# Performance work log

Hardware: AMD Instinct MI355X
Metric: run time of the kernel (lower is better)

The kernel has to match this reference:

```python
import jax, jax.numpy as jnp
import numpy as np

TOPK_FRAC = 0.05  # init arg `topk` (fraction of pool kept)


def setup_inputs() -> dict:
    key = jax.random.key(0)
    k1, k2 = jax.random.split(key)
    x = jax.random.normal(k1, (16, 256, 32, 32), dtype=jnp.float32)
    # nn.Parameter(torch.rand(P, C)) -> uniform [0, 1)
    visual_concept_pool = jax.random.uniform(k2, (2048, 256), dtype=jnp.float32)
    return {"x": x, "visual_concept_pool": visual_concept_pool}


def reference(x, visual_concept_pool):
    n, c, h, w = x.shape
    P = visual_concept_pool.shape[0]
    L = h * w
    xf = x.reshape(n, c, L)                              # [n, c, L]
    # dot_product[n, P, L] = pool @ xf
    dot = jnp.einsum('pc,ncl->npl', visual_concept_pool, xf)
    pool_norm = jnp.sqrt(jnp.sum(visual_concept_pool ** 2, axis=1))   # [P]
    x_norm = jnp.sqrt(jnp.sum(xf ** 2, axis=1))                        # [n, L]
    cos = dot / (pool_norm[None, :, None] * x_norm[:, None, :])       # [n, P, L]

    # mode 1.1: top-k over the pool dimension per (n, pixel)
    keep = int(TOPK_FRAC * P)
    cos_t = jnp.transpose(cos, (0, 2, 1))                # [n, L, P]
    _, idx = jax.lax.top_k(jnp.abs(cos_t), keep)         # [n, L, keep]
    mask = jnp.zeros_like(cos_t).at[
        jnp.arange(n)[:, None, None],
        jnp.arange(L)[None, :, None],
        idx,
    ].set(1.0)                                           # [n, L, P]
    masked = cos_t * mask
    normed = masked / jnp.sum(masked, axis=-1, keepdims=True)  # renormalize over P
    # reconstruct[n, c, L] = pool^T @ cos
    recon = jnp.einsum('pc,nlp->ncl', visual_concept_pool, normed)
    return recon.reshape(n, c, h, w)
```

## Files before the change

### kernel.cpp

```cpp
#include <hip/hip_runtime.h>
#include <hip/hip_fp16.h>

typedef unsigned short u16;
typedef _Float16 half8 __attribute__((ext_vector_type(8)));
typedef float floatx4 __attribute__((ext_vector_type(4)));

#define C_DIM 256
#define P_DIM 2048
#define L_DIM 1024
#define N_DIM 16
#define KEEP 102
#define KPAD 104
#define HALF_PIX 8192
#define SCALE 256.0f

__device__ __forceinline__ void st8(u16* dst, const u16* s) {
  uint4 u;
  u.x = (unsigned)s[0] | ((unsigned)s[1] << 16);
  u.y = (unsigned)s[2] | ((unsigned)s[3] << 16);
  u.z = (unsigned)s[4] | ((unsigned)s[5] << 16);
  u.w = (unsigned)s[6] | ((unsigned)s[7] << 16);
  *(uint4*)dst = u;
}

__device__ __forceinline__ u16 f2h_ftz(float v) {
  if (fabsf(v) < 6.103515625e-5f) return 0;
  return __half_as_ushort(__float2half(v));
}

__device__ __forceinline__ void gl_lds16(const u16* g, u16* l) {
  __builtin_amdgcn_global_load_lds(
      (const __attribute__((address_space(1))) unsigned int*)g,
      (__attribute__((address_space(3))) unsigned int*)l, 16, 0, 0);
}

__global__ __launch_bounds__(256) void k_pinv(const float* __restrict__ pool,
                                              float* __restrict__ pinv) {
  int p = blockIdx.x * 256 + threadIdx.x;
  const float4* row = (const float4*)(pool + (size_t)p * C_DIM);
  float s = 0.f;
#pragma unroll
  for (int i = 0; i < C_DIM / 4; ++i) {
    float4 v = row[i];
    s += v.x * v.x + v.y * v.y + v.z * v.z + v.w * v.w;
  }
  pinv[p] = 1.0f / sqrtf(s);
}

__global__ __launch_bounds__(256) void k_packpool(const float* __restrict__ pool,
                                                  const float* __restrict__ pinv,
                                                  u16* __restrict__ ah,
                                                  u16* __restrict__ al,
                                                  u16* __restrict__ ph) {
  int tid = blockIdx.x * 256 + threadIdx.x;
  int lane = tid & 63;
  int ks = (tid >> 6) & 7;
  int pm = tid >> 9;
  int p = pm * 16 + (lane & 15);
  int c0 = ks * 32 + ((lane >> 4) << 3);
  float sc = pinv[p] * SCALE;
  const float* src = pool + (size_t)p * C_DIM + c0;
  u16 h8[8], l8[8], p8[8];
#pragma unroll
  for (int j = 0; j < 8; ++j) {
    float raw = src[j];
    p8[j] = __half_as_ushort(__float2half(raw));
    float v = raw * sc;
    u16 h = f2h_ftz(v);
    float r = v - __half2float(__ushort_as_half(h));
    h8[j] = h;
    l8[j] = f2h_ftz(r);
  }
  size_t o = (size_t)tid * 8;
  st8(ah + o, h8); st8(al + o, l8);
  st8(ph + (size_t)p * C_DIM + c0, p8);
}

__global__ __launch_bounds__(256) void k_packx(const float* __restrict__ x,
                                               u16* __restrict__ xh,
                                               u16* __restrict__ xl) {
  int tid = blockIdx.x * 256 + threadIdx.x;
  int lane = tid & 63;
  int ks = (tid >> 6) & 7;
  int pn = tid >> 9;
  int pix = pn * 16 + (lane & 15);
  int n = pix >> 10, l = pix & 1023;
  int c0 = ks * 32 + ((lane >> 4) << 3);
  const float* src = x + ((size_t)(n * C_DIM + c0)) * L_DIM + l;
  u16 h8[8], l8[8];
#pragma unroll
  for (int j = 0; j < 8; ++j) {
    float v = src[(size_t)j * L_DIM] * SCALE;
    u16 h = f2h_ftz(v);
    float r = v - __half2float(__ushort_as_half(h));
    h8[j] = h;
    l8[j] = f2h_ftz(r);
  }
  size_t o = (size_t)tid * 8;
  st8(xh + o, h8); st8(xl + o, l8);
}

__global__ __launch_bounds__(256, 4) void k_mfma(const u16* __restrict__ ah_,
                                                 const u16* __restrict__ al_,
                                                 const u16* __restrict__ xh_,
                                                 const u16* __restrict__ xl_,
                                                 float* __restrict__ sbuf,
                                                 int half) {
  __shared__ u16 sB[2][2][8][512];

  const int t = threadIdx.x, lane = t & 63, w = t >> 6;
  const int pT = blockIdx.x & 15, pixT = blockIdx.x >> 4;
  const int pmBase = pT * 8 + w * 2;
  const int pnBase = half * 512 + pixT * 8;
  const half8* A8h = (const half8*)ah_;
  const half8* A8l = (const half8*)al_;

  const u16* xsrc[2] = {xh_, xl_};

  floatx4 acc[2][8];
#pragma unroll
  for (int mt = 0; mt < 2; ++mt)
#pragma unroll
    for (int nt = 0; nt < 8; ++nt) acc[mt][nt] = (floatx4){0.f, 0.f, 0.f, 0.f};

#pragma unroll
  for (int q = 0; q < 4; ++q) {
    int id = w * 4 + q;
    int arr = id >> 3, nt = id & 7;
    const u16* g = xsrc[arr] + ((size_t)(pnBase + nt) * 512 + lane) * 8;
    gl_lds16(g, &sB[0][arr][nt][0]);
  }
  __syncthreads();

#pragma unroll 1
  for (int ks = 0; ks < 8; ++ks) {
    const int cur = ks & 1;
    half8 aH[2], aL[2];
    const size_t ao = (size_t)ks * 64 + lane;
#pragma unroll
    for (int mt = 0; mt < 2; ++mt) {
      size_t idx = (size_t)(pmBase + mt) * 512 + ao;
      aH[mt] = A8h[idx]; aL[mt] = A8l[idx];
    }
    if (ks < 7) {
#pragma unroll
      for (int q = 0; q < 4; ++q) {
        int id = w * 4 + q;
        int arr = id >> 3, nt = id & 7;
        const u16* g = xsrc[arr] + ((size_t)(pnBase + nt) * 512 + (ks + 1) * 64 + lane) * 8;
        gl_lds16(g, &sB[cur ^ 1][arr][nt][0]);
      }
    }
#pragma unroll
    for (int nt = 0; nt < 8; ++nt) {
      half8 bh = *(const half8*)&sB[cur][0][nt][lane * 8];
      half8 bl = *(const half8*)&sB[cur][1][nt][lane * 8];
#pragma unroll
      for (int mt = 0; mt < 2; ++mt) {
        floatx4 c = acc[mt][nt];
        c = __builtin_amdgcn_mfma_f32_16x16x32_f16(aH[mt], bh, c, 0, 0, 0);
        c = __builtin_amdgcn_mfma_f32_16x16x32_f16(aH[mt], bl, c, 0, 0, 0);
        c = __builtin_amdgcn_mfma_f32_16x16x32_f16(aL[mt], bh, c, 0, 0, 0);
        acc[mt][nt] = c;
      }
    }
    __syncthreads();
  }

  const int qr = lane >> 4, cl = lane & 15;
  const int pix0 = pixT * 128;
  const int pbase = pT * 128 + w * 32;
#pragma unroll
  for (int mt = 0; mt < 2; ++mt)
#pragma unroll
    for (int nt = 0; nt < 8; ++nt) {
      float* dst = sbuf + (size_t)(pix0 + nt * 16 + cl) * P_DIM + pbase + mt * 16 + qr * 4;
      *(float4*)dst = make_float4(acc[mt][nt][0], acc[mt][nt][1],
                                  acc[mt][nt][2], acc[mt][nt][3]);
    }
}

__global__ __launch_bounds__(512) void k_select(const float* __restrict__ sbuf,
                                                const u16* __restrict__ pool_h,
                                                float* __restrict__ out,
                                                int half) {
  __shared__ __align__(16) float tbuf[8][260];
  __shared__ int2 kpw[8][KPAD];

  const int t = threadIdx.x;
  const int lane = t & 63;
  const int wv = t >> 6;
  const int b = blockIdx.x;
  const int gp0 = half * HALF_PIX + b * 8;
  const int n = gp0 >> 10;
  const int l0 = gp0 & 1023;
  const float* sp = sbuf + (size_t)(b * 8 + wv) * P_DIM;

  float4 v[8];
#pragma unroll
  for (int q = 0; q < 8; ++q) v[q] = *(const float4*)(sp + q * 256 + lane * 4);

  if (lane < KPAD - KEEP) kpw[wv][KEEP + lane] = make_int2(0, 0);

  float M = 0.f;
#pragma unroll
  for (int q = 0; q < 8; ++q) {
    M = fmaxf(M, fabsf(v[q].x)); M = fmaxf(M, fabsf(v[q].y));
    M = fmaxf(M, fabsf(v[q].z)); M = fmaxf(M, fabsf(v[q].w));
  }
#pragma unroll
  for (int off = 1; off < 64; off <<= 1) M = fmaxf(M, __shfl_xor(M, off));
  const unsigned bitsM = __float_as_uint(M);

  unsigned lo = 0u, hi = bitsM + 1u;
  unsigned m = (bitsM > (5u << 23)) ? (bitsM - (5u << 23)) : ((lo + hi) >> 1);
  while (hi - lo > 1u) {
    float mf = __uint_as_float(m);
    unsigned cnt = 0;
#pragma unroll
    for (int q = 0; q < 8; ++q) {
      cnt += (unsigned)__popcll(__ballot(fabsf(v[q].x) >= mf));
      cnt += (unsigned)__popcll(__ballot(fabsf(v[q].y) >= mf));
      cnt += (unsigned)__popcll(__ballot(fabsf(v[q].z) >= mf));
      cnt += (unsigned)__popcll(__ballot(fabsf(v[q].w) >= mf));
    }
    if (cnt >= KEEP) lo = m; else hi = m;
    m = lo + ((hi - lo) >> 1);
  }
  const float V = __uint_as_float(lo);
  const float Vp = __uint_as_float(lo + 1u);

  unsigned gt = 0;
#pragma unroll
  for (int q = 0; q < 8; ++q) {
    gt += (unsigned)__popcll(__ballot(fabsf(v[q].x) >= Vp));
    gt += (unsigned)__popcll(__ballot(fabsf(v[q].y) >= Vp));
    gt += (unsigned)__popcll(__ballot(fabsf(v[q].z) >= Vp));
    gt += (unsigned)__popcll(__ballot(fabsf(v[q].w) >= Vp));
  }
  const unsigned rrem = (unsigned)KEEP - gt;

  unsigned gmask[8], tmask[8];
#pragma unroll
  for (int q = 0; q < 8; ++q) {
    const float* f = (const float*)&v[q];
    unsigned gm = 0, tm = 0;
#pragma unroll
    for (int rr = 0; rr < 4; ++rr) {
      float av = fabsf(f[rr]);
      if (av >= Vp) gm |= (1u << rr);
      else if (av >= V) tm |= (1u << rr);
    }
    gmask[q] = gm; tmask[q] = tm;
  }

  const unsigned long long lowm = (1ull << lane) - 1ull;
  unsigned base = 0, tiebase = 0;
  float Ssum = 0.f;
#pragma unroll
  for (int q = 0; q < 8; ++q) {
    const float* f = (const float*)&v[q];
    unsigned teq = 0, myeqb = 0;
#pragma unroll
    for (int rr = 0; rr < 4; ++rr) {
      unsigned long long beq = __ballot((tmask[q] >> rr) & 1u);
      teq += (unsigned)__popcll(beq);
      myeqb += (unsigned)__popcll(beq & lowm);
    }
    unsigned km = gmask[q];
    {
      unsigned cum = 0;
#pragma unroll
      for (int rr = 0; rr < 4; ++rr) {
        if ((tmask[q] >> rr) & 1u) {
          if (tiebase + myeqb + cum < rrem) km |= (1u << rr);
          ++cum;
        }
      }
    }
    unsigned long long bk[4];
    unsigned tot = 0, myb = 0;
#pragma unroll
    for (int rr = 0; rr < 4; ++rr) {
      bk[rr] = __ballot((km >> rr) & 1u);
      tot += (unsigned)__popcll(bk[rr]);
      myb += (unsigned)__popcll(bk[rr] & lowm);
    }
    {
      unsigned cum = 0;
#pragma unroll
      for (int rr = 0; rr < 4; ++rr) {
        if ((km >> rr) & 1u) {
          unsigned pos = base + myb + cum;
          kpw[wv][pos] = make_int2(q * 256 + lane * 4 + rr, __float_as_int(f[rr]));
          Ssum += f[rr];
          ++cum;
        }
      }
    }
    base += tot;
    tiebase += teq;
  }

#pragma unroll
  for (int off = 1; off < 64; off <<= 1) Ssum += __shfl_xor(Ssum, off);
  const float invS = 1.0f / Ssum;

  __builtin_amdgcn_wave_barrier();

  float a0 = 0.f, a1 = 0.f, a2 = 0.f, a3 = 0.f;
  const u16* pb = pool_h + 4 * lane;
  int2 e[4];
  uint2 r[4];
#pragma unroll
  for (int j = 0; j < 4; ++j) e[j] = kpw[wv][j];
#pragma unroll
  for (int j = 0; j < 4; ++j) r[j] = *(const uint2*)(pb + (size_t)e[j].x * C_DIM);
  for (int k = 0; k < KPAD; k += 4) {
    int kn = (k + 4 < KPAD) ? k + 4 : 0;
    int2 en[4];
    uint2 rn[4];
#pragma unroll
    for (int j = 0; j < 4; ++j) en[j] = kpw[wv][kn + j];
#pragma unroll
    for (int j = 0; j < 4; ++j) rn[j] = *(const uint2*)(pb + (size_t)en[j].x * C_DIM);
#pragma unroll
    for (int j = 0; j < 4; ++j) {
      float w = __int_as_float(e[j].y);
      float f0 = __half2float(__ushort_as_half((u16)(r[j].x & 0xffffu)));
      float f1 = __half2float(__ushort_as_half((u16)(r[j].x >> 16)));
      float f2 = __half2float(__ushort_as_half((u16)(r[j].y & 0xffffu)));
      float f3 = __half2float(__ushort_as_half((u16)(r[j].y >> 16)));
      a0 = fmaf(w, f0, a0); a1 = fmaf(w, f1, a1);
      a2 = fmaf(w, f2, a2); a3 = fmaf(w, f3, a3);
    }
#pragma unroll
    for (int j = 0; j < 4; ++j) { e[j] = en[j]; r[j] = rn[j]; }
  }
  a0 *= invS; a1 *= invS; a2 *= invS; a3 *= invS;

  *(float4*)&tbuf[wv][4 * lane] = make_float4(a0, a1, a2, a3);
  __syncthreads();

  {
    int c = t >> 1, lq = t & 1;
    float4 o = make_float4(tbuf[4 * lq + 0][c], tbuf[4 * lq + 1][c],
                           tbuf[4 * lq + 2][c], tbuf[4 * lq + 3][c]);
    *(float4*)(out + ((size_t)(n * C_DIM + c)) * L_DIM + l0 + 4 * lq) = o;
  }
}

extern "C" void kernel_launch(void* const* d_in, const int* in_sizes, int n_in,
                              void* d_out, int out_size, void* d_ws, size_t ws_size,
                              hipStream_t stream) {
  const float* x = (const float*)d_in[0];
  const float* pool = (const float*)d_in[1];
  float* out = (float*)d_out;
  char* wsb = (char*)d_ws;
  float* sbuf = (float*)wsb;
  u16* xh = (u16*)(wsb + 67108864);
  u16* xl = xh + 4194304;
  u16* ah = xl + 4194304;
  u16* al = ah + 524288;
  u16* ph = al + 524288;
  float* pinv = (float*)(ph + 524288);

  k_pinv<<<P_DIM / 256, 256, 0, stream>>>(pool, pinv);
  k_packpool<<<256, 256, 0, stream>>>(pool, pinv, ah, al, ph);
  k_packx<<<2048, 256, 0, stream>>>(x, xh, xl);
  for (int h = 0; h < 2; ++h) {
    k_mfma<<<1024, 256, 0, stream>>>(ah, al, xh, xl, sbuf, h);
    k_select<<<1024, 512, 0, stream>>>(sbuf, ph, out, h);
  }
}
```

Baseline: 269.8 us.

## Fuse GEMM and top-k select into one pipelined kernel over pixel quarters

Merges the MFMA cosine GEMM and the top-k select/reconstruct kernels into a single kernel whose blocks are split between computing GEMM for one pixel quarter and running selection on the previous quarter, using two score buffers. This overlaps the compute-bound matrix work with the memory- and latency-bound selection instead of serializing them. MFMA blocks now use 8 waves each holding one m-tile, and the reconstruction loop uses v_fma_mix_f32 inline asm to fuse the half-to-float conversion into the FMA. Shared memory is unioned between the two roles, and the larger block may change occupancy and register pressure.

```diff
diff --git a/kernel.cpp b/kernel.cpp
--- a/kernel.cpp
+++ b/kernel.cpp
@@ -11,7 +11,7 @@
 #define N_DIM 16
 #define KEEP 102
 #define KPAD 104
-#define HALF_PIX 8192
+#define QTR_PIX 4096
 #define SCALE 256.0f
 
 __device__ __forceinline__ void st8(u16* dst, const u16* s) {
@@ -33,6 +33,11 @@
       (const __attribute__((address_space(1))) unsigned int*)g,
       (__attribute__((address_space(3))) unsigned int*)l, 16, 0, 0);
 }
+
+union SMem {
+  u16 sB[2][2][8][512];
+  struct { float tbuf[8][260]; int2 kpw[8][KPAD]; } sel;
+};
 
 __global__ __launch_bounds__(256) void k_pinv(const float* __restrict__ pool,
                                               float* __restrict__ pinv) {
@@ -100,98 +105,84 @@
   st8(xh + o, h8); st8(xl + o, l8);
 }
 
-__global__ __launch_bounds__(256, 4) void k_mfma(const u16* __restrict__ ah_,
-                                                 const u16* __restrict__ al_,
-                                                 const u16* __restrict__ xh_,
-                                                 const u16* __restrict__ xl_,
-                                                 float* __restrict__ sbuf,
-                                                 int half) {
-  __shared__ u16 sB[2][2][8][512];
-
+__device__ __forceinline__ void mfma_body(int b, int mq,
+                                          const u16* __restrict__ ah_,
+                                          const u16* __restrict__ al_,
+                                          const u16* __restrict__ xh_,
+                                          const u16* __restrict__ xl_,
+                                          float* __restrict__ sbuf,
+                                          u16 (*sB)[2][8][512]) {
   const int t = threadIdx.x, lane = t & 63, w = t >> 6;
-  const int pT = blockIdx.x & 15, pixT = blockIdx.x >> 4;
-  const int pmBase = pT * 8 + w * 2;
-  const int pnBase = half * 512 + pixT * 8;
+  const int pT = b & 15, pixT = b >> 4;
+  const int pm = pT * 8 + w;
+  const int pnBase = mq * 256 + pixT * 8;
   const half8* A8h = (const half8*)ah_;
   const half8* A8l = (const half8*)al_;
-
   const u16* xsrc[2] = {xh_, xl_};
 
-  floatx4 acc[2][8];
-#pragma unroll
-  for (int mt = 0; mt < 2; ++mt)
-#pragma unroll
-    for (int nt = 0; nt < 8; ++nt) acc[mt][nt] = (floatx4){0.f, 0.f, 0.f, 0.f};
-
-#pragma unroll
-  for (int q = 0; q < 4; ++q) {
-    int id = w * 4 + q;
+  floatx4 acc[8];
+#pragma unroll
+  for (int nt = 0; nt < 8; ++nt) acc[nt] = (floatx4){0.f, 0.f, 0.f, 0.f};
+
+#pragma unroll
+  for (int q = 0; q < 2; ++q) {
+    int id = w * 2 + q;
     int arr = id >> 3, nt = id & 7;
-    const u16* g = xsrc[arr] + ((size_t)(pnBase + nt) * 512 + lane) * 8;
-    gl_lds16(g, &sB[0][arr][nt][0]);
+    gl_lds16(xsrc[arr] + ((size_t)(pnBase + nt) * 512 + lane) * 8,
+             &sB[0][arr][nt][0]);
   }
   __syncthreads();
 
 #pragma unroll 1
   for (int ks = 0; ks < 8; ++ks) {
     const int cur = ks & 1;
-    half8 aH[2], aL[2];
-    const size_t ao = (size_t)ks * 64 + lane;
-#pragma unroll
-    for (int mt = 0; mt < 2; ++mt) {
-      size_t idx = (size_t)(pmBase + mt) * 512 + ao;
-      aH[mt] = A8h[idx]; aL[mt] = A8l[idx];
+    half8 aH, aL;
+    {
+      size_t idx = (size_t)pm * 512 + (size_t)ks * 64 + lane;
+      aH = A8h[idx]; aL = A8l[idx];
     }
     if (ks < 7) {
 #pragma unroll
-      for (int q = 0; q < 4; ++q) {
-        int id = w * 4 + q;
+      for (int q = 0; q < 2; ++q) {
+        int id = w * 2 + q;
         int arr = id >> 3, nt = id & 7;
-        const u16* g = xsrc[arr] + ((size_t)(pnBase + nt) * 512 + (ks + 1) * 64 + lane) * 8;
-        gl_lds16(g, &sB[cur ^ 1][arr][nt][0]);
+        gl_lds16(xsrc[arr] + ((size_t)(pnBase + nt) * 512 + (ks + 1) * 64 + lane) * 8,
+                 &sB[cur ^ 1][arr][nt][0]);
       }
     }
 #pragma unroll
     for (int nt = 0; nt < 8; ++nt) {
       half8 bh = *(const half8*)&sB[cur][0][nt][lane * 8];
       half8 bl = *(const half8*)&sB[cur][1][nt][lane * 8];
-#pragma unroll
-      for (int mt = 0; mt < 2; ++mt) {
-        floatx4 c = acc[mt][nt];
-        c = __builtin_amdgcn_mfma_f32_16x16x32_f16(aH[mt], bh, c, 0, 0, 0);
-        c = __builtin_amdgcn_mfma_f32_16x16x32_f16(aH[mt], bl, c, 0, 0, 0);
-        c = __builtin_amdgcn_mfma_f32_16x16x32_f16(aL[mt], bh, c, 0, 0, 0);
-        acc[mt][nt] = c;
-      }
+      floatx4 c = acc[nt];
+      c = __builtin_amdgcn_mfma_f32_16x16x32_f16(aH, bh, c, 0, 0, 0);
+      c = __builtin_amdgcn_mfma_f32_16x16x32_f16(aH, bl, c, 0, 0, 0);
+      c = __builtin_amdgcn_mfma_f32_16x16x32_f16(aL, bh, c, 0, 0, 0);
+      acc[nt] = c;
     }
     __syncthreads();
   }
 
   const int qr = lane >> 4, cl = lane & 15;
   const int pix0 = pixT * 128;
-  const int pbase = pT * 128 + w * 32;
-#pragma unroll
-  for (int mt = 0; mt < 2; ++mt)
-#pragma unroll
-    for (int nt = 0; nt < 8; ++nt) {
-      float* dst = sbuf + (size_t)(pix0 + nt * 16 + cl) * P_DIM + pbase + mt * 16 + qr * 4;
-      *(float4*)dst = make_float4(acc[mt][nt][0], acc[mt][nt][1],
-                                  acc[mt][nt][2], acc[mt][nt][3]);
-    }
-}
-
-__global__ __launch_bounds__(512) void k_select(const float* __restrict__ sbuf,
-                                                const u16* __restrict__ pool_h,
-                                                float* __restrict__ out,
-                                                int half) {
-  __shared__ __align__(16) float tbuf[8][260];
-  __shared__ int2 kpw[8][KPAD];
-
+  const int pcol = pT * 128 + w * 16;
+#pragma unroll
+  for (int nt = 0; nt < 8; ++nt) {
+    float* dst = sbuf + (size_t)(pix0 + nt * 16 + cl) * P_DIM + pcol + qr * 4;
+    *(float4*)dst = make_float4(acc[nt][0], acc[nt][1], acc[nt][2], acc[nt][3]);
+  }
+}
+
+__device__ __forceinline__ void select_body(int b, int sq,
+                                            const float* __restrict__ sbuf,
+                                            const u16* __restrict__ pool_h,
+                                            float* __restrict__ out,
+                                            float (*tbuf)[260],
+                                            int2 (*kpw)[KPAD]) {
   const int t = threadIdx.x;
   const int lane = t & 63;
   const int wv = t >> 6;
-  const int b = blockIdx.x;
-  const int gp0 = half * HALF_PIX + b * 8;
+  const int gp0 = sq * QTR_PIX + b * 8;
   const int n = gp0 >> 10;
   const int l0 = gp0 & 1023;
   const float* sp = sbuf + (size_t)(b * 8 + wv) * P_DIM;
@@ -326,13 +317,16 @@
     for (int j = 0; j < 4; ++j) rn[j] = *(const uint2*)(pb + (size_t)en[j].x * C_DIM);
 #pragma unroll
     for (int j = 0; j < 4; ++j) {
-      float w = __int_as_float(e[j].y);
-      float f0 = __half2float(__ushort_as_half((u16)(r[j].x & 0xffffu)));
-      float f1 = __half2float(__ushort_as_half((u16)(r[j].x >> 16)));
-      float f2 = __half2float(__ushort_as_half((u16)(r[j].y & 0xffffu)));
-      float f3 = __half2float(__ushort_as_half((u16)(r[j].y >> 16)));
-      a0 = fmaf(w, f0, a0); a1 = fmaf(w, f1, a1);
-      a2 = fmaf(w, f2, a2); a3 = fmaf(w, f3, a3);
+      float w2 = __int_as_float(e[j].y);
+      unsigned rx = r[j].x, ry = r[j].y;
+      asm volatile("v_fma_mix_f32 %0, %1, %2, %0 op_sel:[0,0,0] op_sel_hi:[0,1,0]"
+                   : "+v"(a0) : "v"(w2), "v"(rx));
+      asm volatile("v_fma_mix_f32 %0, %1, %2, %0 op_sel:[0,1,0] op_sel_hi:[0,1,0]"
+                   : "+v"(a1) : "v"(w2), "v"(rx));
+      asm volatile("v_fma_mix_f32 %0, %1, %2, %0 op_sel:[0,0,0] op_sel_hi:[0,1,0]"
+                   : "+v"(a2) : "v"(w2), "v"(ry));
+      asm volatile("v_fma_mix_f32 %0, %1, %2, %0 op_sel:[0,1,0] op_sel_hi:[0,1,0]"
+                   : "+v"(a3) : "v"(w2), "v"(ry));
     }
 #pragma unroll
     for (int j = 0; j < 4; ++j) { e[j] = en[j]; r[j] = rn[j]; }
@@ -347,6 +341,25 @@
     float4 o = make_float4(tbuf[4 * lq + 0][c], tbuf[4 * lq + 1][c],
                            tbuf[4 * lq + 2][c], tbuf[4 * lq + 3][c]);
     *(float4*)(out + ((size_t)(n * C_DIM + c)) * L_DIM + l0 + 4 * lq) = o;
+  }
+}
+
+__global__ __launch_bounds__(512, 4) void k_main(const u16* __restrict__ ah_,
+                                                 const u16* __restrict__ al_,
+                                                 const u16* __restrict__ xh_,
+                                                 const u16* __restrict__ xl_,
+                                                 const u16* __restrict__ ph,
+                                                 float* __restrict__ sbuf0,
+                                                 float* __restrict__ sbuf1,
+                                                 float* __restrict__ out,
+                                                 int mq, int sq) {
+  __shared__ __align__(16) SMem sm;
+  const int b = blockIdx.x;
+  const int nsel = (sq >= 0) ? 512 : 0;
+  if (b < nsel) {
+    select_body(b, sq, (sq & 1) ? sbuf1 : sbuf0, ph, out, sm.sel.tbuf, sm.sel.kpw);
+  } else {
+    mfma_body(b - nsel, mq, ah_, al_, xh_, xl_, (mq & 1) ? sbuf1 : sbuf0, sm.sB);
   }
 }
 
@@ -357,7 +370,8 @@
   const float* pool = (const float*)d_in[1];
   float* out = (float*)d_out;
   char* wsb = (char*)d_ws;
-  float* sbuf = (float*)wsb;
+  float* sbuf0 = (float*)wsb;
+  float* sbuf1 = (float*)(wsb + 33554432);
   u16* xh = (u16*)(wsb + 67108864);
   u16* xl = xh + 4194304;
   u16* ah = xl + 4194304;
@@ -368,8 +382,10 @@
   k_pinv<<<P_DIM / 256, 256, 0, stream>>>(pool, pinv);
   k_packpool<<<256, 256, 0, stream>>>(pool, pinv, ah, al, ph);
   k_packx<<<2048, 256, 0, stream>>>(x, xh, xl);
-  for (int h = 0; h < 2; ++h) {
-    k_mfma<<<1024, 256, 0, stream>>>(ah, al, xh, xl, sbuf, h);
-    k_select<<<1024, 512, 0, stream>>>(sbuf, ph, out, h);
-  }
-}
+
+  k_main<<<512, 512, 0, stream>>>(ah, al, xh, xl, ph, sbuf0, sbuf1, out, 0, -1);
+  k_main<<<1024, 512, 0, stream>>>(ah, al, xh, xl, ph, sbuf0, sbuf1, out, 1, 0);
+  k_main<<<1024, 512, 0, stream>>>(ah, al, xh, xl, ph, sbuf0, sbuf1, out, 2, 1);
+  k_main<<<1024, 512, 0, stream>>>(ah, al, xh, xl, ph, sbuf0, sbuf1, out, 3, 2);
+  k_main<<<512, 512, 0, stream>>>(ah, al, xh, xl, ph, sbuf0, sbuf1, out, -1, 3);
+}
```

Result: no change. 270.1 us (+0.1%).
